# Performance work log

Hardware: AMD Instinct MI355X
Metric: run time of the kernel (lower is better)

## Reference

```python
import jax, jax.numpy as jnp
import numpy as np

K = 3
PAD = 1
DIL = 1
EPS = 1e-5


def _conv2d(x, w, b=None, pad=1):
    y = jax.lax.conv_general_dilated(x, w, (1, 1), [(pad, pad), (pad, pad)],
                                     dimension_numbers=('NCHW', 'OIHW', 'NCHW'))
    if b is not None:
        y = y + b[None, :, None, None]
    return y


def _conv_transpose(x, w, stride=2, pad=1):
    # torch ConvTranspose2d(k=4, s=2, p=1): lhs-dilated conv with flipped, transposed kernel
    kh = w.shape[2]
    w_t = jnp.flip(w, (2, 3)).transpose(1, 0, 2, 3)  # [in,out,kh,kw] -> [out,in,kh,kw]
    p = kh - 1 - pad
    return jax.lax.conv_general_dilated(x, w_t, (1, 1), [(p, p), (p, p)],
                                        lhs_dilation=(stride, stride),
                                        dimension_numbers=('NCHW', 'OIHW', 'NCHW'))


def _bn(x, g, b):
    # BatchNorm2d training-mode forward (batch stats, biased var)
    m = x.mean(axis=(0, 2, 3), keepdims=True)
    v = x.var(axis=(0, 2, 3), keepdims=True)
    return (x - m) * jax.lax.rsqrt(v + EPS) * g[None, :, None, None] + b[None, :, None, None]


def _deform_conv(x, off_x, off_y, mask, w):
    # Modulated deformable conv v2, stride=1, pad=K//2, groups=1, deform_groups=1
    B, C, H, W = x.shape
    K2 = K * K
    ky, kx = jnp.meshgrid(jnp.arange(K), jnp.arange(K), indexing='ij')
    base_y = (ky.reshape(-1) * DIL - PAD).astype(x.dtype)  # [K2]
    base_x = (kx.reshape(-1) * DIL - PAD).astype(x.dtype)
    hh = jnp.arange(H, dtype=x.dtype)
    ww = jnp.arange(W, dtype=x.dtype)
    # sampling coords per kernel tap: [B, K2, H, W]
    sy = off_y + base_y[None, :, None, None] + hh[None, None, :, None]
    sx = off_x + base_x[None, :, None, None] + ww[None, None, None, :]
    y0 = jnp.floor(sy)
    x0 = jnp.floor(sx)
    ly = sy - y0
    lx = sx - x0
    xf = x.reshape(B, C, H * W)

    def corner(yi, xi, wgt):
        valid = ((yi >= 0) & (yi < H) & (xi >= 0) & (xi < W)).astype(x.dtype)
        idx = (jnp.clip(yi, 0, H - 1) * W + jnp.clip(xi, 0, W - 1)).astype(jnp.int32)
        idx = idx.reshape(B, K2, H * W)
        v = jnp.take_along_axis(xf[:, :, None, :], idx[:, None, :, :], axis=3)  # [B,C,K2,HW]
        return v * (wgt * valid).reshape(B, 1, K2, H * W)

    val = (corner(y0, x0, (1 - ly) * (1 - lx)) + corner(y0, x0 + 1, (1 - ly) * lx)
           + corner(y0 + 1, x0, ly * (1 - lx)) + corner(y0 + 1, x0 + 1, ly * lx))
    val = val * mask.reshape(B, 1, K2, H * W)  # modulation
    O = w.shape[0]
    out = jnp.einsum('bip,oi->bop', val.reshape(B, C * K2, H * W), w.reshape(O, C * K2))
    return out.reshape(B, O, H, W)


def setup_inputs() -> dict:
    key = jax.random.key(0)
    ks = jax.random.split(key, 6)
    B, C, H, W, O = 4, 256, 64, 64, 256
    x = jax.random.normal(ks[0], (B, C, H, W), jnp.float32)
    w_off = jax.random.normal(ks[1], (3 * K * K, C, K, K), jnp.float32) * 0.01
    b_off = jax.random.normal(ks[2], (3 * K * K,), jnp.float32) * 0.01
    w_dcn = jax.random.normal(ks[3], (O, C, K, K), jnp.float32) * float(np.sqrt(2.0 / (C * K * K)))
    w_up = jax.random.normal(ks[4], (O, O, 4, 4), jnp.float32) * 0.02
    gamma1 = jnp.ones((O,), jnp.float32)
    beta1 = jnp.zeros((O,), jnp.float32)
    gamma2 = jnp.ones((O,), jnp.float32)
    beta2 = jnp.zeros((O,), jnp.float32)
    return dict(x=x, w_off=w_off, b_off=b_off, w_dcn=w_dcn, gamma1=gamma1, beta1=beta1,
                w_up=w_up, gamma2=gamma2, beta2=beta2)


def reference(x, w_off, b_off, w_dcn, gamma1, beta1, w_up, gamma2, beta2):
    offset_mask = _conv2d(x, w_off, b_off, pad=K // 2)
    off_x, off_y, mask = jnp.split(offset_mask, 3, axis=1)
    mask = jax.nn.sigmoid(mask)
    y = _deform_conv(x, off_x, off_y, mask, w_dcn)
    y = jax.nn.relu(_bn(y, gamma1, beta1))
    y_up = _conv_transpose(y, w_up)
    y_up = jax.nn.relu(_bn(y_up, gamma2, beta2))
    return (y, y_up)
```

## Files before the change

### kernel.cpp

```cpp
#include <hip/hip_runtime.h>
#include <math.h>

#define BB 4
#define CC 256
#define OC 256
#define HH 64
#define WW2 64
#define HW 4096
#define UP_HW 16384
#define NOFF 27
#define EPSV 1e-5f
#define TPX 32

typedef _Float16 f16;
typedef f16 f16x2 __attribute__((ext_vector_type(2)));
typedef f16 f16x4 __attribute__((ext_vector_type(4)));
typedef f16 f16x8 __attribute__((ext_vector_type(8)));
typedef float f32x4 __attribute__((ext_vector_type(4)));

#define GLOAD16(GP, LP) __builtin_amdgcn_global_load_lds( \
    (const __attribute__((address_space(1))) void*)(GP),  \
    (__attribute__((address_space(3))) void*)(LP), 16, 0, 0)

__global__ __launch_bounds__(256) void k_offset(
    const float* __restrict__ x, const float* __restrict__ w,
    const float* __restrict__ bias, float* __restrict__ om) {
  const int b = blockIdx.z;
  const int ocg = blockIdx.y * 3;
  const int row = threadIdx.x >> 6;
  const int h = blockIdx.x * 4 + row;
  const int col = threadIdx.x & 63;
  const float* xb = x + (size_t)b * CC * HW;
  float a0 = 0.f, a1 = 0.f, a2 = 0.f;
  for (int ic = 0; ic < CC; ++ic) {
    const float* xc = xb + ic * HW;
    float xm[3], xl[3], xr[3];
    #pragma unroll
    for (int dy = 0; dy < 3; ++dy) {
      int hy = h + dy - 1;
      float v = (hy >= 0 && hy < HH) ? xc[hy * WW2 + col] : 0.f;
      xm[dy] = v;
      float up = __shfl_up(v, 1, 64);
      float dn = __shfl_down(v, 1, 64);
      xl[dy] = (col == 0) ? 0.f : up;
      xr[dy] = (col == 63) ? 0.f : dn;
    }
    #pragma unroll
    for (int j = 0; j < 3; ++j) {
      const float* wp = w + ((size_t)(ocg + j) * CC + ic) * 9;
      float s = 0.f;
      #pragma unroll
      for (int dy = 0; dy < 3; ++dy) {
        s = fmaf(wp[dy * 3 + 0], xl[dy], s);
        s = fmaf(wp[dy * 3 + 1], xm[dy], s);
        s = fmaf(wp[dy * 3 + 2], xr[dy], s);
      }
      if (j == 0) a0 += s; else if (j == 1) a1 += s; else a2 += s;
    }
  }
  #pragma unroll
  for (int j = 0; j < 3; ++j) {
    int oc = ocg + j;
    float v = (j == 0 ? a0 : (j == 1 ? a1 : a2)) + bias[oc];
    if (oc >= 18) v = 1.f / (1.f + expf(-v));
    om[((size_t)(b * NOFF + oc)) * HW + h * WW2 + col] = v;
  }
}

__global__ __launch_bounds__(256) void k_dcn(
    const float* __restrict__ x, const float* __restrict__ om,
    const float* __restrict__ wd, float* __restrict__ out) {
  __shared__ int s_idx[4][TPX * 9];
  __shared__ float s_bw[4][TPX * 9];
  __shared__ __align__(16) float s_v[2][TPX * 9];
  __shared__ __align__(16) float s_wd[2][9][256];
  const int b = blockIdx.y;
  const int p0 = blockIdx.x * TPX;
  const int h = p0 >> 6;
  const int tid = threadIdx.x;

  for (int e = tid; e < TPX * 9; e += 256) {
    int px = e & (TPX - 1);
    int k = e >> 5;
    int p = p0 + px;
    int wc = p & 63;
    float offx = om[((size_t)(b * NOFF + k)) * HW + p];
    float offy = om[((size_t)(b * NOFF + 9 + k)) * HW + p];
    float msk  = om[((size_t)(b * NOFF + 18 + k)) * HW + p];
    float sy = offy + (float)(k / 3 - 1) + (float)h;
    float sx = offx + (float)(k % 3 - 1) + (float)wc;
    float fy = floorf(sy), fx = floorf(sx);
    float ly = sy - fy, lx = sx - fx;
    int iy = (int)fy, ix = (int)fx;
    #pragma unroll
    for (int cnr = 0; cnr < 4; ++cnr) {
      int dy = cnr >> 1, dx = cnr & 1;
      int yy = iy + dy, xx = ix + dx;
      bool val = (yy >= 0) & (yy < HH) & (xx >= 0) & (xx < WW2);
      float wt = (dy ? ly : 1.f - ly) * (dx ? lx : 1.f - lx) * msk;
      s_idx[cnr][e] = val ? (yy * WW2 + xx) : 0;
      s_bw[cnr][e] = val ? wt : 0.f;
    }
  }
  __syncthreads();

  const int og = tid >> 3, pg = tid & 7;
  float acc[8][4] = {};
  const float* xb = x + (size_t)b * CC * HW;
  for (int ic = 0; ic < CC; ic += 2) {
    {
      const float* wp = wd + (size_t)tid * (CC * 9) + ic * 9;
      #pragma unroll
      for (int t = 0; t < 18; ++t)
        s_wd[t / 9][t % 9][tid] = wp[t];
    }
    #pragma unroll
    for (int t = 0; t < 3; ++t) {
      int e = tid + t * 256;
      if (e < 2 * TPX * 9) {
        int icc = (e >= TPX * 9);
        int r = e - icc * TPX * 9;
        const float* xc = xb + (ic + icc) * HW;
        float v = s_bw[0][r] * xc[s_idx[0][r]] + s_bw[1][r] * xc[s_idx[1][r]]
                + s_bw[2][r] * xc[s_idx[2][r]] + s_bw[3][r] * xc[s_idx[3][r]];
        s_v[icc][r] = v;
      }
    }
    __syncthreads();
    #pragma unroll
    for (int icc = 0; icc < 2; ++icc) {
      #pragma unroll
      for (int k = 0; k < 9; ++k) {
        float4 v4 = *(const float4*)&s_v[icc][k * TPX + pg * 4];
        float4 wa = *(const float4*)&s_wd[icc][k][og * 8];
        float4 wb = *(const float4*)&s_wd[icc][k][og * 8 + 4];
        float vi[4] = {v4.x, v4.y, v4.z, v4.w};
        float wj[8] = {wa.x, wa.y, wa.z, wa.w, wb.x, wb.y, wb.z, wb.w};
        #pragma unroll
        for (int j = 0; j < 8; ++j)
          #pragma unroll
          for (int i = 0; i < 4; ++i)
            acc[j][i] = fmaf(wj[j], vi[i], acc[j][i]);
      }
    }
    __syncthreads();
  }
  #pragma unroll
  for (int j = 0; j < 8; ++j) {
    int oc = og * 8 + j;
    float4 o = make_float4(acc[j][0], acc[j][1], acc[j][2], acc[j][3]);
    *(float4*)&out[((size_t)(b * OC + oc)) * HW + p0 + pg * 4] = o;
  }
}

__global__ __launch_bounds__(256) void k_stats(
    const float* __restrict__ d, int perB, float* __restrict__ mean,
    float* __restrict__ rinv) {
  const int c = blockIdx.x, tid = threadIdx.x;
  double s1 = 0.0, s2 = 0.0;
  const int n4 = perB >> 2;
  for (int b = 0; b < BB; ++b) {
    const float4* p = (const float4*)(d + ((size_t)(b * CC + c)) * perB);
    for (int i = tid; i < n4; i += 256) {
      float4 v = p[i];
      s1 += (double)v.x + (double)v.y + (double)v.z + (double)v.w;
      s2 += (double)v.x * v.x + (double)v.y * v.y + (double)v.z * v.z + (double)v.w * v.w;
    }
  }
  __shared__ double r1[256], r2[256];
  r1[tid] = s1; r2[tid] = s2;
  __syncthreads();
  for (int s = 128; s > 0; s >>= 1) {
    if (tid < s) { r1[tid] += r1[tid + s]; r2[tid] += r2[tid + s]; }
    __syncthreads();
  }
  if (tid == 0) {
    double n = (double)perB * BB;
    double m = r1[0] / n;
    double var = r2[0] / n - m * m;
    mean[c] = (float)m;
    rinv[c] = (float)(1.0 / sqrt(var + (double)EPSV));
  }
}

__global__ __launch_bounds__(256) void k_stats_part(
    const float* __restrict__ d, int perB, double* __restrict__ part) {
  const int c = blockIdx.x & 255, b = blockIdx.x >> 8;
  const int tid = threadIdx.x;
  double s1 = 0.0, s2 = 0.0;
  const float4* p = (const float4*)(d + ((size_t)(b * CC + c)) * perB);
  const int n4 = perB >> 2;
  for (int i = tid; i < n4; i += 256) {
    float4 v = p[i];
    s1 += (double)v.x + (double)v.y + (double)v.z + (double)v.w;
    s2 += (double)v.x * v.x + (double)v.y * v.y + (double)v.z * v.z + (double)v.w * v.w;
  }
  __shared__ double r1[256], r2[256];
  r1[tid] = s1; r2[tid] = s2;
  __syncthreads();
  for (int s = 128; s > 0; s >>= 1) {
    if (tid < s) { r1[tid] += r1[tid + s]; r2[tid] += r2[tid + s]; }
    __syncthreads();
  }
  if (tid == 0) {
    part[blockIdx.x] = r1[0];
    part[1024 + blockIdx.x] = r2[0];
  }
}

__global__ __launch_bounds__(256) void k_stats_fin(
    const double* __restrict__ part, int perB, float* __restrict__ mean,
    float* __restrict__ rinv) {
  const int c = threadIdx.x;
  double s1 = 0.0, s2 = 0.0;
  #pragma unroll
  for (int b = 0; b < BB; ++b) {
    s1 += part[b * 256 + c];
    s2 += part[1024 + b * 256 + c];
  }
  double n = (double)perB * BB;
  double m = s1 / n;
  double var = s2 / n - m * m;
  mean[c] = (float)m;
  rinv[c] = (float)(1.0 / sqrt(var + (double)EPSV));
}

__global__ __launch_bounds__(256) void k_bnrelu(
    float* __restrict__ d, const float* __restrict__ mean,
    const float* __restrict__ rinv, const float* __restrict__ g,
    const float* __restrict__ be, int perB, int total4) {
  int stride = gridDim.x * blockDim.x;
  for (int i4 = blockIdx.x * blockDim.x + threadIdx.x; i4 < total4; i4 += stride) {
    int c = (int)((((long long)i4 * 4) / perB) & 255);
    float sc = rinv[c] * g[c];
    float shv = fmaf(-mean[c], sc, be[c]);
    float4 v = ((float4*)d)[i4];
    v.x = fmaxf(fmaf(v.x, sc, shv), 0.f);
    v.y = fmaxf(fmaf(v.y, sc, shv), 0.f);
    v.z = fmaxf(fmaf(v.z, sc, shv), 0.f);
    v.w = fmaxf(fmaf(v.w, sc, shv), 0.f);
    ((float4*)d)[i4] = v;
  }
}

__global__ __launch_bounds__(256) void k_totile(const float* __restrict__ y,
                                                f16* __restrict__ yTp) {
  __shared__ float S[32][33];
  const int h = blockIdx.x;
  const int cg = blockIdx.y >> 1;
  const int wg = blockIdx.y & 1;
  const int b = blockIdx.z;
  const int t = threadIdx.x;
  {
    int ci = t >> 3, q = t & 7;
    const float* src = y + (((size_t)(b * 256 + cg * 32 + ci) * 64 + h) * 64 + wg * 32 + q * 4);
    float4 v = *(const float4*)src;
    S[ci][q * 4 + 0] = v.x; S[ci][q * 4 + 1] = v.y;
    S[ci][q * 4 + 2] = v.z; S[ci][q * 4 + 3] = v.w;
  }
  __syncthreads();
  {
    int w = t >> 3, c2 = t & 7;
    f16x4 pv;
    pv[0] = (f16)S[c2 * 4 + 0][w];
    pv[1] = (f16)S[c2 * 4 + 1][w];
    pv[2] = (f16)S[c2 * 4 + 2][w];
    pv[3] = (f16)S[c2 * 4 + 3][w];
    f16* dst = yTp + (((size_t)(b * 66 + h + 1) * 66 + (wg * 32 + w + 1)) * 256 + cg * 32 + c2 * 4);
    *(f16x4*)dst = pv;
  }
}

__global__ __launch_bounds__(256) void k_totile_bn(
    const float* __restrict__ mean, const float* __restrict__ rinv,
    const float* __restrict__ g, const float* __restrict__ be,
    float* __restrict__ y, f16* __restrict__ yTp) {
  __shared__ float S[32][33];
  const int h = blockIdx.x;
  const int cg = blockIdx.y >> 1;
  const int wg = blockIdx.y & 1;
  const int b = blockIdx.z;
  const int t = threadIdx.x;
  {
    int ci = t >> 3, q = t & 7;
    int c = cg * 32 + ci;
    float sc = rinv[c] * g[c];
    float sh = fmaf(-mean[c], sc, be[c]);
    float* src = y + (((size_t)(b * 256 + c) * 64 + h) * 64 + wg * 32 + q * 4);
    float4 v = *(const float4*)src;
    v.x = fmaxf(fmaf(v.x, sc, sh), 0.f);
    v.y = fmaxf(fmaf(v.y, sc, sh), 0.f);
    v.z = fmaxf(fmaf(v.z, sc, sh), 0.f);
    v.w = fmaxf(fmaf(v.w, sc, sh), 0.f);
    *(float4*)src = v;
    S[ci][q * 4 + 0] = v.x; S[ci][q * 4 + 1] = v.y;
    S[ci][q * 4 + 2] = v.z; S[ci][q * 4 + 3] = v.w;
  }
  __syncthreads();
  {
    int w = t >> 3, c2 = t & 7;
    f16x4 pv;
    pv[0] = (f16)S[c2 * 4 + 0][w];
    pv[1] = (f16)S[c2 * 4 + 1][w];
    pv[2] = (f16)S[c2 * 4 + 2][w];
    pv[3] = (f16)S[c2 * 4 + 3][w];
    f16* dst = yTp + (((size_t)(b * 66 + h + 1) * 66 + (wg * 32 + w + 1)) * 256 + cg * 32 + c2 * 4);
    *(f16x4*)dst = pv;
  }
}

__global__ __launch_bounds__(128) void k_pad0(f16* __restrict__ p0,
                                              f16* __restrict__ p1) {
  f16* base = blockIdx.z ? p1 : p0;
  const int j = blockIdx.x;
  const int b = blockIdx.y;
  int row, col;
  if (j < 66)       { row = 0;      col = j; }
  else if (j < 132) { row = 65;     col = j - 66; }
  else if (j < 196) { row = j - 131; col = 0; }
  else              { row = j - 195; col = 65; }
  unsigned int* p = (unsigned int*)&base[(((size_t)b * 66 + row) * 66 + col) * 256];
  p[threadIdx.x] = 0u;
}

__global__ __launch_bounds__(256) void k_wdprep(const float* __restrict__ wd,
                                                f16* __restrict__ Wd) {
  const int oc = blockIdx.x, ic = threadIdx.x;
  const float* src = wd + ((size_t)oc * 256 + ic) * 9;
  f16* dst = Wd + (((size_t)(ic >> 3) * 256 + oc)) * 8 + (ic & 7);
  #pragma unroll
  for (int tap = 0; tap < 9; ++tap)
    dst[(size_t)tap * 32 * 256 * 8] = (f16)src[tap];
}

__global__ __launch_bounds__(256) void k_wodprep(const float* __restrict__ wo,
                                                 f16* __restrict__ Wod) {
  const int oc = blockIdx.x;
  const int ic = threadIdx.x;
  const int icg = ic >> 3, e = ic & 7;
  #pragma unroll
  for (int tap = 0; tap < 9; ++tap) {
    f16 v = (f16)0.f;
    if (oc < NOFF) v = (f16)wo[((size_t)oc * 256 + ic) * 9 + tap];
    Wod[(((size_t)(tap * 32 + icg)) * 32 + oc) * 8 + e] = v;
  }
}

__global__ __launch_bounds__(256) void k_off_mfma(
    const f16* __restrict__ xtp, const f16* __restrict__ Wod,
    const float* __restrict__ bias, float* __restrict__ om) {
  __shared__ __align__(16) f16 Alds[9 * 4 * 32 * 8];
  __shared__ __align__(16) f16 Blds[6 * 4 * 66 * 8];
  const int b = blockIdx.y;
  const int r0 = blockIdx.x * 4;
  const int tid = threadIdx.x;
  const int lane = tid & 63, wave = tid >> 6;
  const int l15 = lane & 15, l4 = lane >> 4;
  f32x4 acc[2][4] = {};
  const size_t xbase = ((size_t)b * 66 + r0) * 66;

  for (int ic0 = 0; ic0 < 256; ic0 += 32) {
    if (ic0) __syncthreads();
    #pragma unroll
    for (int i = 0; i < 5; ++i) {
      int idx = i * 256 + tid;
      if (idx < 1152) {
        int tap = idx >> 7, rem = idx & 127;
        int g = rem >> 5, oc = rem & 31;
        f16x8 v = *(const f16x8*)(Wod + (((size_t)(tap * 32 + (ic0 >> 3) + g)) * 32 + oc) * 8);
        *(f16x8*)&Alds[((tap * 4 + g) * 32 + oc) * 8] = v;
      }
    }
    #pragma unroll
    for (int i = 0; i < 7; ++i) {
      int idx = i * 256 + tid;
      if (idx < 1584) {
        int g = idx & 3, quad = idx >> 2;
        int rp = quad / 66, c = quad - rp * 66;
        f16x8 v = *(const f16x8*)(xtp + ((xbase + rp * 66 + c) * 256 + ic0 + g * 8));
        *(f16x8*)&Blds[((rp * 4 + g) * 66 + c) * 8] = v;
      }
    }
    __syncthreads();
    #pragma unroll
    for (int tap = 0; tap < 9; ++tap) {
      const int ky = tap / 3, kx = tap % 3;
      f16x8 af[2], bf[4];
      #pragma unroll
      for (int fi = 0; fi < 2; ++fi)
        af[fi] = *(const f16x8*)&Alds[((tap * 4 + l4) * 32 + fi * 16 + l15) * 8];
      #pragma unroll
      for (int ni = 0; ni < 4; ++ni)
        bf[ni] = *(const f16x8*)&Blds[(((wave + ky) * 4 + l4) * 66 + ni * 16 + l15 + kx) * 8];
      #pragma unroll
      for (int fi = 0; fi < 2; ++fi)
        #pragma unroll
        for (int ni = 0; ni < 4; ++ni)
          acc[fi][ni] = __builtin_amdgcn_mfma_f32_16x16x32_f16(af[fi], bf[ni], acc[fi][ni], 0, 0, 0);
    }
  }
  #pragma unroll
  for (int fi = 0; fi < 2; ++fi) {
    #pragma unroll
    for (int r = 0; r < 4; ++r) {
      int oc = fi * 16 + l4 * 4 + r;
      if (oc < NOFF) {
        float bv = bias[oc];
        #pragma unroll
        for (int ni = 0; ni < 4; ++ni) {
          int px = (r0 + wave) * 64 + ni * 16 + l15;
          float v = acc[fi][ni][r] + bv;
          if (oc >= 18) v = 1.f / (1.f + expf(-v));
          om[((size_t)(b * NOFF + oc)) * HW + px] = v;
        }
      }
    }
  }
}

__global__ __launch_bounds__(256) void k_sample(
    const f16* __restrict__ xtp, const float* __restrict__ om,
    f16* __restrict__ V, int b0) {
  const int tap = blockIdx.y;
  const int vb = blockIdx.z;
  const int b = b0 + vb;
  const int p = blockIdx.x * 64 + (threadIdx.x & 63);
  const int icg0 = threadIdx.x >> 6;
  const int h = p >> 6, w = p & 63;
  const float offx = om[((size_t)(b * NOFF + tap)) * HW + p];
  const float offy = om[((size_t)(b * NOFF + 9 + tap)) * HW + p];
  const float msk  = om[((size_t)(b * NOFF + 18 + tap)) * HW + p];
  float sy = offy + (float)(tap / 3 - 1) + (float)h;
  float sx = offx + (float)(tap % 3 - 1) + (float)w;
  float fy = floorf(sy), fx = floorf(sx);
  float ly = sy - fy, lx = sx - fx;
  int iy = (int)fy, ix = (int)fx;
  int idx[4];
  float wg[4];
  #pragma unroll
  for (int cnr = 0; cnr < 4; ++cnr) {
    int dy = cnr >> 1, dx = cnr & 1;
    int yy = iy + dy, xx = ix + dx;
    bool val = (yy >= 0) & (yy < HH) & (xx >= 0) & (xx < WW2);
    float wt = (dy ? ly : 1.f - ly) * (dx ? lx : 1.f - lx) * msk;
    idx[cnr] = val ? ((yy + 1) * 66 + (xx + 1)) : 0;
    wg[cnr] = val ? wt : 0.f;
  }
  const f16* xb = xtp + (size_t)b * 66 * 66 * 256;
  f16* vout = V + (((size_t)(vb * 9 + tap) * 32) * HW + p) * 8;
  #pragma unroll
  for (int it = 0; it < 8; ++it) {
    int icg = icg0 + it * 4;
    f16x8 c0 = *(const f16x8*)(xb + (size_t)idx[0] * 256 + icg * 8);
    f16x8 c1 = *(const f16x8*)(xb + (size_t)idx[1] * 256 + icg * 8);
    f16x8 c2 = *(const f16x8*)(xb + (size_t)idx[2] * 256 + icg * 8);
    f16x8 c3 = *(const f16x8*)(xb + (size_t)idx[3] * 256 + icg * 8);
    f16x8 r;
    #pragma unroll
    for (int e = 0; e < 8; ++e) {
      float s = wg[0] * (float)c0[e];
      s = fmaf(wg[1], (float)c1[e], s);
      s = fmaf(wg[2], (float)c2[e], s);
      s = fmaf(wg[3], (float)c3[e], s);
      r[e] = (f16)s;
    }
    *(f16x8*)(vout + (size_t)icg * HW * 8) = r;
  }
}

__global__ __launch_bounds__(256) void k_dcn_mfma(
    const f16* __restrict__ V, const f16* __restrict__ Wd,
    float* __restrict__ out, int b0) {
  __shared__ __align__(16) f16 Alds[8 * 128 * 8];
  __shared__ __align__(16) f16 Blds[8 * 128 * 8];
  const int vb = blockIdx.z;
  const int b = b0 + vb;
  const int oc0 = blockIdx.y * 128;
  const int px0 = blockIdx.x * 128;
  const int tid = threadIdx.x;
  const int lane = tid & 63;
  const int wave = tid >> 6;
  const int wm = wave >> 1, wn = wave & 1;
  const int l15 = lane & 15, l4 = lane >> 4;
  const int wbase = tid & 192;
  f32x4 acc[4][4] = {};

  for (int tap = 0; tap < 9; ++tap) {
    for (int kk = 0; kk < 4; ++kk) {
      __syncthreads();
      #pragma unroll
      for (int i = 0; i < 4; ++i) {
        int idx = i * 256 + tid;
        int g = idx >> 7, q = idx & 127;
        const f16* gpA = Wd + (((size_t)((tap * 32 + kk * 8 + g) * 256) + oc0 + q)) * 8;
        const f16* gpB = V + ((((size_t)(vb * 9 + tap) * 32) + kk * 8 + g) * HW + px0 + q) * 8;
        f16* lpA = Alds + (size_t)(i * 256 + wbase) * 8;
        f16* lpB = Blds + (size_t)(i * 256 + wbase) * 8;
        GLOAD16(gpA, lpA);
        GLOAD16(gpB, lpB);
      }
      __syncthreads();
      #pragma unroll
      for (int half = 0; half < 2; ++half) {
        f16x8 af[4], bf[4];
        #pragma unroll
        for (int fi = 0; fi < 4; ++fi)
          af[fi] = *(const f16x8*)&Alds[(((half * 4 + l4) * 128) + wm * 64 + fi * 16 + l15) * 8];
        #pragma unroll
        for (int ni = 0; ni < 4; ++ni)
          bf[ni] = *(const f16x8*)&Blds[(((half * 4 + l4) * 128) + wn * 64 + ni * 16 + l15) * 8];
        #pragma unroll
        for (int fi = 0; fi < 4; ++fi)
          #pragma unroll
          for (int ni = 0; ni < 4; ++ni)
            acc[fi][ni] = __builtin_amdgcn_mfma_f32_16x16x32_f16(af[fi], bf[ni], acc[fi][ni], 0, 0, 0);
      }
    }
  }
  #pragma unroll
  for (int fi = 0; fi < 4; ++fi) {
    int oc = oc0 + wm * 64 + fi * 16 + l4 * 4;
    #pragma unroll
    for (int ni = 0; ni < 4; ++ni) {
      int px = px0 + wn * 64 + ni * 16 + l15;
      float* op = out + ((size_t)(b * OC + oc)) * HW + px;
      #pragma unroll
      for (int r = 0; r < 4; ++r)
        op[(size_t)r * HW] = acc[fi][ni][r];
    }
  }
}

__global__ __launch_bounds__(256) void k_wprep(const float* __restrict__ wu,
                                               f16* __restrict__ Wt) {
  const int ic = blockIdx.x * 2;
  const int oc = threadIdx.x;
  float a[16], c[16];
  const float* p0 = wu + ((size_t)(ic * 256 + oc)) * 16;
  const float* p1 = wu + ((size_t)((ic + 1) * 256 + oc)) * 16;
  #pragma unroll
  for (int k = 0; k < 4; ++k) {
    float4 v = *(const float4*)(p0 + k * 4);
    a[k * 4 + 0] = v.x; a[k * 4 + 1] = v.y; a[k * 4 + 2] = v.z; a[k * 4 + 3] = v.w;
    float4 w2 = *(const float4*)(p1 + k * 4);
    c[k * 4 + 0] = w2.x; c[k * 4 + 1] = w2.y; c[k * 4 + 2] = w2.z; c[k * 4 + 3] = w2.w;
  }
  #pragma unroll
  for (int kh = 0; kh < 4; ++kh)
    #pragma unroll
    for (int kw = 0; kw < 4; ++kw) {
      int po = (kh & 1) ^ 1, dh = kh >> 1;
      int qo = (kw & 1) ^ 1, dw = kw >> 1;
      int combo = (po * 2 + qo) * 4 + (dh * 2 + dw);
      f16x2 pv;
      pv[0] = (f16)a[kh * 4 + kw];
      pv[1] = (f16)c[kh * 4 + kw];
      *(f16x2*)&Wt[((size_t)(combo * 256 + oc)) * 256 + ic] = pv;
    }
}

__global__ __launch_bounds__(256) void k_up_mfma(
    const f16* __restrict__ yTp, const f16* __restrict__ Wt,
    float* __restrict__ out) {
  __shared__ __align__(16) f16 Alds[4 * 4 * 128 * 8];
  __shared__ __align__(16) f16 Blds[5 * 4 * 66 * 8];
  const int b = blockIdx.z;
  const int sub = blockIdx.y >> 1;
  const int po = sub >> 1, qo = sub & 1;
  const int oc0 = (blockIdx.y & 1) * 128;
  const int sh0 = blockIdx.x * 4;
  const int tid = threadIdx.x;
  const int lane = tid & 63, wave = tid >> 6;
  const int wm = wave >> 1, wn = wave & 1;
  const int l15 = lane & 15, l4 = lane >> 4;
  const int wbase = tid & 192;
  f32x4 acc[4][8] = {};
  const size_t yrow = ((size_t)b * 66 + (sh0 + po)) * 66;

  for (int ic0 = 0; ic0 < 256; ic0 += 32) {
    __syncthreads();
    #pragma unroll
    for (int i = 0; i < 8; ++i) {
      int idx = i * 256 + tid;
      int tap = idx >> 9, g = (idx >> 7) & 3, oc = idx & 127;
      const f16* gp = Wt + (((size_t)((sub * 4 + tap) * 256 + oc0 + oc)) * 256 + ic0 + g * 8);
      GLOAD16(gp, Alds + (size_t)(i * 256 + wbase) * 8);
    }
    #pragma unroll
    for (int i = 0; i < 6; ++i) {
      int idx = i * 256 + tid;
      if (idx < 1320) {
        int rp4g = idx / 66, c = idx - rp4g * 66;
        int rp = rp4g >> 2, g = rp4g & 3;
        const f16* gp = yTp + ((yrow + rp * 66 + c) * 256 + ic0 + g * 8);
        GLOAD16(gp, Blds + (size_t)(i * 256 + wbase) * 8);
      }
    }
    __syncthreads();
    #pragma unroll
    for (int tap = 0; tap < 4; ++tap) {
      const int dh = tap >> 1, dw = tap & 1;
      f16x8 af[4];
      #pragma unroll
      for (int fi = 0; fi < 4; ++fi)
        af[fi] = *(const f16x8*)&Alds[((tap * 4 + l4) * 128 + wm * 64 + fi * 16 + l15) * 8];
      #pragma unroll
      for (int ni = 0; ni < 8; ++ni) {
        int px = wn * 128 + ni * 16 + l15;
        int prow = px >> 6;
        int cp = (px & 63) + qo - dw + 1;
        f16x8 bf = *(const f16x8*)&Blds[(((prow + 1 - dh) * 4 + l4) * 66 + cp) * 8];
        #pragma unroll
        for (int fi = 0; fi < 4; ++fi)
          acc[fi][ni] = __builtin_amdgcn_mfma_f32_16x16x32_f16(af[fi], bf, acc[fi][ni], 0, 0, 0);
      }
    }
  }
  #pragma unroll
  for (int fi = 0; fi < 4; ++fi) {
    int oc = oc0 + wm * 64 + fi * 16 + l4 * 4;
    #pragma unroll
    for (int ni = 0; ni < 8; ++ni) {
      int px = wn * 128 + ni * 16 + l15;
      int sh = sh0 + (px >> 6);
      int ow = 2 * (px & 63) + qo;
      float* op = out + ((size_t)(b * 256 + oc)) * UP_HW + (2 * sh + po) * 128 + ow;
      #pragma unroll
      for (int r = 0; r < 4; ++r)
        op[(size_t)r * UP_HW] = acc[fi][ni][r];
    }
  }
}

extern "C" void kernel_launch(void* const* d_in, const int* in_sizes, int n_in,
                              void* d_out, int out_size, void* d_ws, size_t ws_size,
                              hipStream_t stream) {
  const float* x      = (const float*)d_in[0];
  const float* w_off  = (const float*)d_in[1];
  const float* b_off  = (const float*)d_in[2];
  const float* w_dcn  = (const float*)d_in[3];
  const float* gamma1 = (const float*)d_in[4];
  const float* beta1  = (const float*)d_in[5];
  const float* w_up   = (const float*)d_in[6];
  const float* gamma2 = (const float*)d_in[7];
  const float* beta2  = (const float*)d_in[8];

  float* out1 = (float*)d_out;
  float* out2 = out1 + (size_t)BB * OC * HW;

  char* wsb = (char*)d_ws;
  float* om    = (float*)wsb;
  float* mean1 = (float*)(wsb + 1769472);
  float* rinv1 = mean1 + 256;
  float* mean2 = rinv1 + 256;
  float* rinv2 = mean2 + 256;
  f16* yTp = (f16*)(wsb + 1773568);
  f16* Wt  = (f16*)(wsb + 10694656);
  f16* xtp = (f16*)(wsb + 12791808);
  f16* Wd  = (f16*)(wsb + 21712896);
  f16* Wod = (f16*)(wsb + 22892544);
  f16* V   = (f16*)(wsb + 23040000);
  const size_t FIXED_END = 23040000;
  const size_t VB_BYTES = 18874368;

  int nb = 0;
  if (ws_size >= FIXED_END + 4 * VB_BYTES) nb = 4;
  else if (ws_size >= FIXED_END + 2 * VB_BYTES) nb = 2;
  else if (ws_size >= FIXED_END + VB_BYTES) nb = 1;

  hipLaunchKernelGGL(k_wprep, dim3(128), dim3(256), 0, stream, w_up, Wt);

  if (nb > 0) {
    double* partd = (double*)V;
    hipLaunchKernelGGL(k_pad0, dim3(260, BB, 2), dim3(128), 0, stream, yTp, xtp);
    hipLaunchKernelGGL(k_totile, dim3(64, 16, BB), dim3(256), 0, stream, x, xtp);
    hipLaunchKernelGGL(k_wodprep, dim3(32), dim3(256), 0, stream, w_off, Wod);
    hipLaunchKernelGGL(k_wdprep, dim3(256), dim3(256), 0, stream, w_dcn, Wd);
    hipLaunchKernelGGL(k_off_mfma, dim3(16, BB), dim3(256), 0, stream, xtp, Wod, b_off, om);
    for (int b0 = 0; b0 < BB; b0 += nb) {
      hipLaunchKernelGGL(k_sample, dim3(64, 9, nb), dim3(256), 0, stream, xtp, om, V, b0);
      hipLaunchKernelGGL(k_dcn_mfma, dim3(32, 2, nb), dim3(256), 0, stream, V, Wd, out1, b0);
    }
    hipLaunchKernelGGL(k_stats_part, dim3(1024), dim3(256), 0, stream, out1, HW, partd);
    hipLaunchKernelGGL(k_stats_fin, dim3(1), dim3(256), 0, stream, partd, HW, mean1, rinv1);
    hipLaunchKernelGGL(k_totile_bn, dim3(64, 16, BB), dim3(256), 0, stream,
                       mean1, rinv1, gamma1, beta1, out1, yTp);
    hipLaunchKernelGGL(k_up_mfma, dim3(16, 8, BB), dim3(256), 0, stream, yTp, Wt, out2);
    hipLaunchKernelGGL(k_stats_part, dim3(1024), dim3(256), 0, stream, out2, UP_HW, partd);
    hipLaunchKernelGGL(k_stats_fin, dim3(1), dim3(256), 0, stream, partd, UP_HW, mean2, rinv2);
  } else {
    hipLaunchKernelGGL(k_pad0, dim3(260, BB, 1), dim3(128), 0, stream, yTp, yTp);
    hipLaunchKernelGGL(k_offset, dim3(16, 9, BB), dim3(256), 0, stream, x, w_off, b_off, om);
    hipLaunchKernelGGL(k_dcn, dim3(HW / TPX, BB), dim3(256), 0, stream, x, om, w_dcn, out1);
    hipLaunchKernelGGL(k_stats, dim3(256), dim3(256), 0, stream, out1, HW, mean1, rinv1);
    hipLaunchKernelGGL(k_bnrelu, dim3(2048), dim3(256), 0, stream, out1, mean1, rinv1,
                       gamma1, beta1, HW, (BB * OC * HW) / 4);
    hipLaunchKernelGGL(k_totile, dim3(64, 16, BB), dim3(256), 0, stream, out1, yTp);
    hipLaunchKernelGGL(k_up_mfma, dim3(16, 8, BB), dim3(256), 0, stream, yTp, Wt, out2);
    hipLaunchKernelGGL(k_stats, dim3(256), dim3(256), 0, stream, out2, UP_HW, mean2, rinv2);
  }

  hipLaunchKernelGGL(k_bnrelu, dim3(2048), dim3(256), 0, stream, out2, mean2, rinv2,
                     gamma2, beta2, UP_HW, (BB * OC * UP_HW) / 4);
}
```

Before: 228.2 us.

## Fuse BN statistics into GEMM epilogues and retile offset conv per row

The DCN and transposed-conv MFMA kernels now reduce per-channel sum and sum-of-squares in their epilogues and write float partials. A single-block finisher combines them, replacing the separate stats pass that re-read out1 and out2. The offset-conv kernel is retiled to one output row per block, giving four times as many blocks, and its LDS staging now uses direct global-to-LDS loads. The cost is extra epilogue work, float rather than double partial accumulation, and a fused path that runs only when the workspace is large enough for four batches.

```diff
diff --git a/kernel.cpp b/kernel.cpp
--- a/kernel.cpp
+++ b/kernel.cpp
@@ -217,6 +217,24 @@
   for (int b = 0; b < BB; ++b) {
     s1 += part[b * 256 + c];
     s2 += part[1024 + b * 256 + c];
+  }
+  double n = (double)perB * BB;
+  double m = s1 / n;
+  double var = s2 / n - m * m;
+  mean[c] = (float)m;
+  rinv[c] = (float)(1.0 / sqrt(var + (double)EPSV));
+}
+
+__global__ __launch_bounds__(256) void k_stats_fin_f(
+    const float* __restrict__ part, int P, int perB, float* __restrict__ mean,
+    float* __restrict__ rinv) {
+  const int c = threadIdx.x;
+  double s1 = 0.0, s2 = 0.0;
+  const float* p1 = part + (size_t)c * P;
+  const float* p2 = part + (size_t)256 * P + (size_t)c * P;
+  for (int i = 0; i < P; ++i) {
+    s1 += (double)p1[i];
+    s2 += (double)p2[i];
   }
   double n = (double)perB * BB;
   double m = s1 / n;
@@ -350,69 +368,60 @@
     const f16* __restrict__ xtp, const f16* __restrict__ Wod,
     const float* __restrict__ bias, float* __restrict__ om) {
   __shared__ __align__(16) f16 Alds[9 * 4 * 32 * 8];
-  __shared__ __align__(16) f16 Blds[6 * 4 * 66 * 8];
+  __shared__ __align__(16) f16 Blds[3 * 4 * 66 * 8];
   const int b = blockIdx.y;
-  const int r0 = blockIdx.x * 4;
+  const int r = blockIdx.x;
   const int tid = threadIdx.x;
   const int lane = tid & 63, wave = tid >> 6;
   const int l15 = lane & 15, l4 = lane >> 4;
-  f32x4 acc[2][4] = {};
-  const size_t xbase = ((size_t)b * 66 + r0) * 66;
+  const int wbase = tid & 192;
+  f32x4 acc[2] = {};
+  const size_t xbase = ((size_t)b * 66 + r) * 66;
 
   for (int ic0 = 0; ic0 < 256; ic0 += 32) {
-    if (ic0) __syncthreads();
+    __syncthreads();
     #pragma unroll
     for (int i = 0; i < 5; ++i) {
       int idx = i * 256 + tid;
       if (idx < 1152) {
-        int tap = idx >> 7, rem = idx & 127;
-        int g = rem >> 5, oc = rem & 31;
-        f16x8 v = *(const f16x8*)(Wod + (((size_t)(tap * 32 + (ic0 >> 3) + g)) * 32 + oc) * 8);
-        *(f16x8*)&Alds[((tap * 4 + g) * 32 + oc) * 8] = v;
-      }
-    }
-    #pragma unroll
-    for (int i = 0; i < 7; ++i) {
+        int tap = idx >> 7, g = (idx >> 5) & 3, oc = idx & 31;
+        const f16* gp = Wod + (((size_t)(tap * 32 + (ic0 >> 3) + g)) * 32 + oc) * 8;
+        GLOAD16(gp, Alds + (size_t)(i * 256 + wbase) * 8);
+      }
+    }
+    #pragma unroll
+    for (int i = 0; i < 4; ++i) {
       int idx = i * 256 + tid;
-      if (idx < 1584) {
-        int g = idx & 3, quad = idx >> 2;
-        int rp = quad / 66, c = quad - rp * 66;
-        f16x8 v = *(const f16x8*)(xtp + ((xbase + rp * 66 + c) * 256 + ic0 + g * 8));
-        *(f16x8*)&Blds[((rp * 4 + g) * 66 + c) * 8] = v;
+      if (idx < 792) {
+        int rp4g = idx / 66, c = idx - rp4g * 66;
+        int rp = rp4g >> 2, g = rp4g & 3;
+        const f16* gp = xtp + ((xbase + rp * 66 + c) * 256 + ic0 + g * 8);
+        GLOAD16(gp, Blds + (size_t)(i * 256 + wbase) * 8);
       }
     }
     __syncthreads();
     #pragma unroll
     for (int tap = 0; tap < 9; ++tap) {
       const int ky = tap / 3, kx = tap % 3;
-      f16x8 af[2], bf[4];
+      f16x8 af[2];
       #pragma unroll
       for (int fi = 0; fi < 2; ++fi)
         af[fi] = *(const f16x8*)&Alds[((tap * 4 + l4) * 32 + fi * 16 + l15) * 8];
-      #pragma unroll
-      for (int ni = 0; ni < 4; ++ni)
-        bf[ni] = *(const f16x8*)&Blds[(((wave + ky) * 4 + l4) * 66 + ni * 16 + l15 + kx) * 8];
+      f16x8 bf = *(const f16x8*)&Blds[((ky * 4 + l4) * 66 + wave * 16 + l15 + kx) * 8];
       #pragma unroll
       for (int fi = 0; fi < 2; ++fi)
-        #pragma unroll
-        for (int ni = 0; ni < 4; ++ni)
-          acc[fi][ni] = __builtin_amdgcn_mfma_f32_16x16x32_f16(af[fi], bf[ni], acc[fi][ni], 0, 0, 0);
+        acc[fi] = __builtin_amdgcn_mfma_f32_16x16x32_f16(af[fi], bf, acc[fi], 0, 0, 0);
     }
   }
   #pragma unroll
   for (int fi = 0; fi < 2; ++fi) {
     #pragma unroll
-    for (int r = 0; r < 4; ++r) {
-      int oc = fi * 16 + l4 * 4 + r;
+    for (int r4 = 0; r4 < 4; ++r4) {
+      int oc = fi * 16 + l4 * 4 + r4;
       if (oc < NOFF) {
-        float bv = bias[oc];
-        #pragma unroll
-        for (int ni = 0; ni < 4; ++ni) {
-          int px = (r0 + wave) * 64 + ni * 16 + l15;
-          float v = acc[fi][ni][r] + bv;
-          if (oc >= 18) v = 1.f / (1.f + expf(-v));
-          om[((size_t)(b * NOFF + oc)) * HW + px] = v;
-        }
+        float v = acc[fi][r4] + bias[oc];
+        if (oc >= 18) v = 1.f / (1.f + expf(-v));
+        om[((size_t)(b * NOFF + oc)) * HW + r * 64 + wave * 16 + l15] = v;
       }
     }
   }
@@ -470,7 +479,7 @@
 
 __global__ __launch_bounds__(256) void k_dcn_mfma(
     const f16* __restrict__ V, const f16* __restrict__ Wd,
-    float* __restrict__ out, int b0) {
+    float* __restrict__ out, int b0, float* __restrict__ part) {
   __shared__ __align__(16) f16 Alds[8 * 128 * 8];
   __shared__ __align__(16) f16 Blds[8 * 128 * 8];
   const int vb = blockIdx.z;
@@ -494,10 +503,8 @@
         int g = idx >> 7, q = idx & 127;
         const f16* gpA = Wd + (((size_t)((tap * 32 + kk * 8 + g) * 256) + oc0 + q)) * 8;
         const f16* gpB = V + ((((size_t)(vb * 9 + tap) * 32) + kk * 8 + g) * HW + px0 + q) * 8;
-        f16* lpA = Alds + (size_t)(i * 256 + wbase) * 8;
-        f16* lpB = Blds + (size_t)(i * 256 + wbase) * 8;
-        GLOAD16(gpA, lpA);
-        GLOAD16(gpB, lpB);
+        GLOAD16(gpA, Alds + (size_t)(i * 256 + wbase) * 8);
+        GLOAD16(gpB, Blds + (size_t)(i * 256 + wbase) * 8);
       }
       __syncthreads();
       #pragma unroll
@@ -527,6 +534,40 @@
       #pragma unroll
       for (int r = 0; r < 4; ++r)
         op[(size_t)r * HW] = acc[fi][ni][r];
+    }
+  }
+  if (part) {
+    __syncthreads();
+    float* R1 = (float*)Alds;
+    float* R2 = R1 + 256;
+    #pragma unroll
+    for (int fi = 0; fi < 4; ++fi)
+      #pragma unroll
+      for (int r = 0; r < 4; ++r) {
+        float s1 = 0.f, s2 = 0.f;
+        #pragma unroll
+        for (int ni = 0; ni < 4; ++ni) {
+          float v = acc[fi][ni][r];
+          s1 += v; s2 = fmaf(v, v, s2);
+        }
+        #pragma unroll
+        for (int m = 1; m < 16; m <<= 1) {
+          s1 += __shfl_xor(s1, m, 64);
+          s2 += __shfl_xor(s2, m, 64);
+        }
+        if (l15 == 0) {
+          int sidx = wn * 128 + wm * 64 + l4 * 16 + fi * 4 + r;
+          R1[sidx] = s1; R2[sidx] = s2;
+        }
+      }
+    __syncthreads();
+    if (tid < 128) {
+      int wm_ = tid >> 6, l4_ = (tid >> 4) & 3, fi_ = (tid >> 2) & 3, r_ = tid & 3;
+      int c = oc0 + wm_ * 64 + fi_ * 16 + l4_ * 4 + r_;
+      int sidx = wm_ * 64 + l4_ * 16 + fi_ * 4 + r_;
+      int pb = blockIdx.x * 4 + b;
+      part[(size_t)c * 128 + pb] = R1[sidx] + R1[128 + sidx];
+      part[(size_t)256 * 128 + (size_t)c * 128 + pb] = R2[sidx] + R2[128 + sidx];
     }
   }
 }
@@ -561,7 +602,7 @@
 
 __global__ __launch_bounds__(256) void k_up_mfma(
     const f16* __restrict__ yTp, const f16* __restrict__ Wt,
-    float* __restrict__ out) {
+    float* __restrict__ out, float* __restrict__ part) {
   __shared__ __align__(16) f16 Alds[4 * 4 * 128 * 8];
   __shared__ __align__(16) f16 Blds[5 * 4 * 66 * 8];
   const int b = blockIdx.z;
@@ -630,6 +671,40 @@
         op[(size_t)r * UP_HW] = acc[fi][ni][r];
     }
   }
+  if (part) {
+    __syncthreads();
+    float* R1 = (float*)Alds;
+    float* R2 = R1 + 256;
+    #pragma unroll
+    for (int fi = 0; fi < 4; ++fi)
+      #pragma unroll
+      for (int r = 0; r < 4; ++r) {
+        float s1 = 0.f, s2 = 0.f;
+        #pragma unroll
+        for (int ni = 0; ni < 8; ++ni) {
+          float v = acc[fi][ni][r];
+          s1 += v; s2 = fmaf(v, v, s2);
+        }
+        #pragma unroll
+        for (int m = 1; m < 16; m <<= 1) {
+          s1 += __shfl_xor(s1, m, 64);
+          s2 += __shfl_xor(s2, m, 64);
+        }
+        if (l15 == 0) {
+          int sidx = wn * 128 + wm * 64 + l4 * 16 + fi * 4 + r;
+          R1[sidx] = s1; R2[sidx] = s2;
+        }
+      }
+    __syncthreads();
+    if (tid < 128) {
+      int wm_ = tid >> 6, l4_ = (tid >> 4) & 3, fi_ = (tid >> 2) & 3, r_ = tid & 3;
+      int c = oc0 + wm_ * 64 + fi_ * 16 + l4_ * 4 + r_;
+      int sidx = wm_ * 64 + l4_ * 16 + fi_ * 4 + r_;
+      int pb = (sub * 16 + blockIdx.x) * 4 + b;
+      part[(size_t)c * 256 + pb] = R1[sidx] + R1[128 + sidx];
+      part[(size_t)256 * 256 + (size_t)c * 256 + pb] = R2[sidx] + R2[128 + sidx];
+    }
+  }
 }
 
 extern "C" void kernel_launch(void* const* d_in, const int* in_sizes, int n_in,
@@ -662,6 +737,8 @@
   f16* V   = (f16*)(wsb + 23040000);
   const size_t FIXED_END = 23040000;
   const size_t VB_BYTES = 18874368;
+  float* part1 = (float*)xtp;
+  float* part2 = (float*)(wsb + 12791808 + 262144);
 
   int nb = 0;
   if (ws_size >= FIXED_END + 4 * VB_BYTES) nb = 4;
@@ -671,23 +748,34 @@
   hipLaunchKernelGGL(k_wprep, dim3(128), dim3(256), 0, stream, w_up, Wt);
 
   if (nb > 0) {
-    double* partd = (double*)V;
     hipLaunchKernelGGL(k_pad0, dim3(260, BB, 2), dim3(128), 0, stream, yTp, xtp);
     hipLaunchKernelGGL(k_totile, dim3(64, 16, BB), dim3(256), 0, stream, x, xtp);
     hipLaunchKernelGGL(k_wodprep, dim3(32), dim3(256), 0, stream, w_off, Wod);
     hipLaunchKernelGGL(k_wdprep, dim3(256), dim3(256), 0, stream, w_dcn, Wd);
-    hipLaunchKernelGGL(k_off_mfma, dim3(16, BB), dim3(256), 0, stream, xtp, Wod, b_off, om);
+    hipLaunchKernelGGL(k_off_mfma, dim3(64, BB), dim3(256), 0, stream, xtp, Wod, b_off, om);
     for (int b0 = 0; b0 < BB; b0 += nb) {
       hipLaunchKernelGGL(k_sample, dim3(64, 9, nb), dim3(256), 0, stream, xtp, om, V, b0);
-      hipLaunchKernelGGL(k_dcn_mfma, dim3(32, 2, nb), dim3(256), 0, stream, V, Wd, out1, b0);
-    }
-    hipLaunchKernelGGL(k_stats_part, dim3(1024), dim3(256), 0, stream, out1, HW, partd);
-    hipLaunchKernelGGL(k_stats_fin, dim3(1), dim3(256), 0, stream, partd, HW, mean1, rinv1);
+      hipLaunchKernelGGL(k_dcn_mfma, dim3(32, 2, nb), dim3(256), 0, stream, V, Wd, out1, b0,
+                         (nb == 4) ? part1 : (float*)nullptr);
+    }
+    if (nb == 4) {
+      hipLaunchKernelGGL(k_stats_fin_f, dim3(1), dim3(256), 0, stream, part1, 128, HW, mean1, rinv1);
+    } else {
+      double* partd = (double*)V;
+      hipLaunchKernelGGL(k_stats_part, dim3(1024), dim3(256), 0, stream, out1, HW, partd);
+      hipLaunchKernelGGL(k_stats_fin, dim3(1), dim3(256), 0, stream, partd, HW, mean1, rinv1);
+    }
     hipLaunchKernelGGL(k_totile_bn, dim3(64, 16, BB), dim3(256), 0, stream,
                        mean1, rinv1, gamma1, beta1, out1, yTp);
-    hipLaunchKernelGGL(k_up_mfma, dim3(16, 8, BB), dim3(256), 0, stream, yTp, Wt, out2);
-    hipLaunchKernelGGL(k_stats_part, dim3(1024), dim3(256), 0, stream, out2, UP_HW, partd);
-    hipLaunchKernelGGL(k_stats_fin, dim3(1), dim3(256), 0, stream, partd, UP_HW, mean2, rinv2);
+    hipLaunchKernelGGL(k_up_mfma, dim3(16, 8, BB), dim3(256), 0, stream, yTp, Wt, out2,
+                       (nb == 4) ? part2 : (float*)nullptr);
+    if (nb == 4) {
+      hipLaunchKernelGGL(k_stats_fin_f, dim3(1), dim3(256), 0, stream, part2, 256, UP_HW, mean2, rinv2);
+    } else {
+      double* partd = (double*)V;
+      hipLaunchKernelGGL(k_stats_part, dim3(1024), dim3(256), 0, stream, out2, UP_HW, partd);
+      hipLaunchKernelGGL(k_stats_fin, dim3(1), dim3(256), 0, stream, partd, UP_HW, mean2, rinv2);
+    }
   } else {
     hipLaunchKernelGGL(k_pad0, dim3(260, BB, 1), dim3(128), 0, stream, yTp, yTp);
     hipLaunchKernelGGL(k_offset, dim3(16, 9, BB), dim3(256), 0, stream, x, w_off, b_off, om);
@@ -696,7 +784,8 @@
     hipLaunchKernelGGL(k_bnrelu, dim3(2048), dim3(256), 0, stream, out1, mean1, rinv1,
                        gamma1, beta1, HW, (BB * OC * HW) / 4);
     hipLaunchKernelGGL(k_totile, dim3(64, 16, BB), dim3(256), 0, stream, out1, yTp);
-    hipLaunchKernelGGL(k_up_mfma, dim3(16, 8, BB), dim3(256), 0, stream, yTp, Wt, out2);
+    hipLaunchKernelGGL(k_up_mfma, dim3(16, 8, BB), dim3(256), 0, stream, yTp, Wt, out2,
+                       (float*)nullptr);
     hipLaunchKernelGGL(k_stats, dim3(256), dim3(256), 0, stream, out2, UP_HW, mean2, rinv2);
   }
 
```

New measurement: 315.3 us. 1.38x slower.

## Split offset conv into one row per block and use direct global-to-LDS loads

Applied to the files above, without the earlier changes.

The offset-conv MFMA kernel now handles one output row per block instead of four, raising the grid from 64 to 256 blocks so more CUs are busy on the MI355X. Each wave computes a 16-pixel slice with two accumulators instead of eight. Tile staging uses global_load_lds (direct global-to-LDS 16-byte loads) instead of going through registers. The trade-off is more redundant loading of weights and halo rows per output and less MFMA work per LDS fill.

```diff
diff --git a/kernel.cpp b/kernel.cpp
--- a/kernel.cpp
+++ b/kernel.cpp
@@ -350,69 +350,60 @@
     const f16* __restrict__ xtp, const f16* __restrict__ Wod,
     const float* __restrict__ bias, float* __restrict__ om) {
   __shared__ __align__(16) f16 Alds[9 * 4 * 32 * 8];
-  __shared__ __align__(16) f16 Blds[6 * 4 * 66 * 8];
+  __shared__ __align__(16) f16 Blds[3 * 4 * 66 * 8];
   const int b = blockIdx.y;
-  const int r0 = blockIdx.x * 4;
+  const int r = blockIdx.x;
   const int tid = threadIdx.x;
   const int lane = tid & 63, wave = tid >> 6;
   const int l15 = lane & 15, l4 = lane >> 4;
-  f32x4 acc[2][4] = {};
-  const size_t xbase = ((size_t)b * 66 + r0) * 66;
+  const int wbase = tid & 192;
+  f32x4 acc[2] = {};
+  const size_t xbase = ((size_t)b * 66 + r) * 66;
 
   for (int ic0 = 0; ic0 < 256; ic0 += 32) {
-    if (ic0) __syncthreads();
+    __syncthreads();
     #pragma unroll
     for (int i = 0; i < 5; ++i) {
       int idx = i * 256 + tid;
       if (idx < 1152) {
-        int tap = idx >> 7, rem = idx & 127;
-        int g = rem >> 5, oc = rem & 31;
-        f16x8 v = *(const f16x8*)(Wod + (((size_t)(tap * 32 + (ic0 >> 3) + g)) * 32 + oc) * 8);
-        *(f16x8*)&Alds[((tap * 4 + g) * 32 + oc) * 8] = v;
-      }
-    }
-    #pragma unroll
-    for (int i = 0; i < 7; ++i) {
+        int tap = idx >> 7, g = (idx >> 5) & 3, oc = idx & 31;
+        const f16* gp = Wod + (((size_t)(tap * 32 + (ic0 >> 3) + g)) * 32 + oc) * 8;
+        GLOAD16(gp, Alds + (size_t)(i * 256 + wbase) * 8);
+      }
+    }
+    #pragma unroll
+    for (int i = 0; i < 4; ++i) {
       int idx = i * 256 + tid;
-      if (idx < 1584) {
-        int g = idx & 3, quad = idx >> 2;
-        int rp = quad / 66, c = quad - rp * 66;
-        f16x8 v = *(const f16x8*)(xtp + ((xbase + rp * 66 + c) * 256 + ic0 + g * 8));
-        *(f16x8*)&Blds[((rp * 4 + g) * 66 + c) * 8] = v;
+      if (idx < 792) {
+        int rp4g = idx / 66, c = idx - rp4g * 66;
+        int rp = rp4g >> 2, g = rp4g & 3;
+        const f16* gp = xtp + ((xbase + rp * 66 + c) * 256 + ic0 + g * 8);
+        GLOAD16(gp, Blds + (size_t)(i * 256 + wbase) * 8);
       }
     }
     __syncthreads();
     #pragma unroll
     for (int tap = 0; tap < 9; ++tap) {
       const int ky = tap / 3, kx = tap % 3;
-      f16x8 af[2], bf[4];
+      f16x8 af[2];
       #pragma unroll
       for (int fi = 0; fi < 2; ++fi)
         af[fi] = *(const f16x8*)&Alds[((tap * 4 + l4) * 32 + fi * 16 + l15) * 8];
-      #pragma unroll
-      for (int ni = 0; ni < 4; ++ni)
-        bf[ni] = *(const f16x8*)&Blds[(((wave + ky) * 4 + l4) * 66 + ni * 16 + l15 + kx) * 8];
+      f16x8 bf = *(const f16x8*)&Blds[((ky * 4 + l4) * 66 + wave * 16 + l15 + kx) * 8];
       #pragma unroll
       for (int fi = 0; fi < 2; ++fi)
-        #pragma unroll
-        for (int ni = 0; ni < 4; ++ni)
-          acc[fi][ni] = __builtin_amdgcn_mfma_f32_16x16x32_f16(af[fi], bf[ni], acc[fi][ni], 0, 0, 0);
+        acc[fi] = __builtin_amdgcn_mfma_f32_16x16x32_f16(af[fi], bf, acc[fi], 0, 0, 0);
     }
   }
   #pragma unroll
   for (int fi = 0; fi < 2; ++fi) {
     #pragma unroll
-    for (int r = 0; r < 4; ++r) {
-      int oc = fi * 16 + l4 * 4 + r;
+    for (int r4 = 0; r4 < 4; ++r4) {
+      int oc = fi * 16 + l4 * 4 + r4;
       if (oc < NOFF) {
-        float bv = bias[oc];
-        #pragma unroll
-        for (int ni = 0; ni < 4; ++ni) {
-          int px = (r0 + wave) * 64 + ni * 16 + l15;
-          float v = acc[fi][ni][r] + bv;
-          if (oc >= 18) v = 1.f / (1.f + expf(-v));
-          om[((size_t)(b * NOFF + oc)) * HW + px] = v;
-        }
+        float v = acc[fi][r4] + bias[oc];
+        if (oc >= 18) v = 1.f / (1.f + expf(-v));
+        om[((size_t)(b * NOFF + oc)) * HW + r * 64 + wave * 16 + l15] = v;
       }
     }
   }
@@ -676,7 +667,7 @@
     hipLaunchKernelGGL(k_totile, dim3(64, 16, BB), dim3(256), 0, stream, x, xtp);
     hipLaunchKernelGGL(k_wodprep, dim3(32), dim3(256), 0, stream, w_off, Wod);
     hipLaunchKernelGGL(k_wdprep, dim3(256), dim3(256), 0, stream, w_dcn, Wd);
-    hipLaunchKernelGGL(k_off_mfma, dim3(16, BB), dim3(256), 0, stream, xtp, Wod, b_off, om);
+    hipLaunchKernelGGL(k_off_mfma, dim3(64, BB), dim3(256), 0, stream, xtp, Wod, b_off, om);
     for (int b0 = 0; b0 < BB; b0 += nb) {
       hipLaunchKernelGGL(k_sample, dim3(64, 9, nb), dim3(256), 0, stream, xtp, om, V, b0);
       hipLaunchKernelGGL(k_dcn_mfma, dim3(32, 2, nb), dim3(256), 0, stream, V, Wd, out1, b0);
```

New measurement: 213.2 us. 6.6% less time.
